# Kernel optimization log

Measured on AMD Instinct MI355X. Metric: run time of the kernel, lower is better.

The kernel has to match this reference:

```python
import jax, jax.numpy as jnp
import numpy as np

D_MODEL = 1024
SEQ_LEN = 32768


def setup_inputs() -> dict:
    key = jax.random.key(0)
    k1, k2, k3 = jax.random.split(key, 3)
    inputs = jax.random.normal(k1, (SEQ_LEN,), dtype=jnp.float32)
    W = jax.random.normal(k2, (D_MODEL, D_MODEL), dtype=jnp.float32) * (1.0 / np.sqrt(D_MODEL))
    b = jax.random.normal(k3, (D_MODEL,), dtype=jnp.float32) * 0.01
    return {"inputs": inputs, "W": W, "b": b}


def reference(inputs, W, b):
    d_model = W.shape[0]
    # t: [D], p: [L] -- log(1 + position)
    t = jnp.linspace(0.0, 1.0, d_model, dtype=inputs.dtype)
    p = jnp.log1p(jnp.arange(inputs.shape[0], dtype=inputs.dtype))
    # phase[l, d] = 2*pi * inputs[l] * (t[d] + p[l]); sum sin over positions
    phase = 2.0 * jnp.pi * inputs[:, None] * (t[None, :] + p[:, None])  # [L, D]
    signal = jnp.sum(jnp.sin(phase), axis=0)  # [D]
    # nn.Linear: x @ W.T + b
    return signal @ W.T + b
```

## Files before the change

### kernel.cpp

```cpp
#include <hip/hip_runtime.h>

#define L_TOTAL 32768
#define D_MODEL 1024
#define CHUNK   128
#define BLOCKS_A (L_TOTAL / CHUNK)

__global__ __launch_bounds__(1024) void signal_kernel(const float* __restrict__ x,
                                                      float* __restrict__ signal) {
    __shared__ float2 sxp[CHUNK];
    const int tid  = threadIdx.x;
    const int base = blockIdx.x * CHUNK;
    if (tid < CHUNK) {
        const float xv = x[base + tid];
        const float pv = __logf(1.0f + (float)(base + tid));
        sxp[tid] = make_float2(xv, xv * pv);
    }
    __syncthreads();

    const float t = (float)tid * (1.0f / 1023.0f);
    float a = 0.f;
    #pragma unroll 8
    for (int il = 0; il < CHUNK; ++il) {
        const float2 v = sxp[il];
        const float g = __builtin_amdgcn_fractf(fmaf(v.x, t, v.y));
        a += __builtin_amdgcn_sinf(g);
    }
    atomicAdd(&signal[tid], a);
}

__global__ __launch_bounds__(256) void matvec_kernel(const float* __restrict__ W,
                                                     const float* __restrict__ b,
                                                     const float* __restrict__ signal,
                                                     float* __restrict__ out) {
    const int wave = threadIdx.x >> 6;
    const int lane = threadIdx.x & 63;
    const int row  = blockIdx.x * 4 + wave;

    const float4* Wr = (const float4*)(W + (size_t)row * D_MODEL);
    const float4* S  = (const float4*)signal;

    float sum = 0.f;
    #pragma unroll
    for (int k = 0; k < 4; ++k) {
        const float4 w4 = Wr[lane + 64 * k];
        const float4 s4 = S[lane + 64 * k];
        sum += w4.x * s4.x + w4.y * s4.y + w4.z * s4.z + w4.w * s4.w;
    }
    #pragma unroll
    for (int off = 32; off > 0; off >>= 1)
        sum += __shfl_down(sum, off, 64);
    if (lane == 0) out[row] = sum + b[row];
}

extern "C" void kernel_launch(void* const* d_in, const int* in_sizes, int n_in,
                              void* d_out, int out_size, void* d_ws, size_t ws_size,
                              hipStream_t stream) {
    const float* x = (const float*)d_in[0];
    const float* W = (const float*)d_in[1];
    const float* b = (const float*)d_in[2];
    float* out    = (float*)d_out;
    float* signal = (float*)d_ws;

    hipMemsetAsync(signal, 0, D_MODEL * sizeof(float), stream);
    signal_kernel<<<BLOCKS_A, 1024, 0, stream>>>(x, signal);
    matvec_kernel<<<D_MODEL / 4, 256, 0, stream>>>(W, b, signal, out);
}
```

Measured before the change: 73.48 us.

## Fuse signal and matvec into one cooperative kernel partitioned by output column

Replaces the memset, the atomic-accumulating signal kernel and the separate matvec kernel with a single cooperative kernel. Each block owns 4 output dimensions and loops over the whole sequence, so the sum needs no atomics, and grid syncs hand the signal vector to the matvec phase through the output buffer. The goal is to remove launch overhead and atomic contention. In exchange, every block recomputes log1p for all positions, two grid-wide barriers are added, and only 4 dims per block limits the parallel work.

```diff
diff --git a/kernel.cpp b/kernel.cpp
--- a/kernel.cpp
+++ b/kernel.cpp
@@ -1,55 +1,89 @@
 #include <hip/hip_runtime.h>
+#include <hip/hip_cooperative_groups.h>
+
+namespace cg = cooperative_groups;
 
 #define L_TOTAL 32768
 #define D_MODEL 1024
-#define CHUNK   128
-#define BLOCKS_A (L_TOTAL / CHUNK)
+#define NBLK    256
+#define NTHR    1024
+#define CL      4096
+#define NCHUNK  (L_TOTAL / CL)
+#define JITER   (CL / 256)
 
-__global__ __launch_bounds__(1024) void signal_kernel(const float* __restrict__ x,
-                                                      float* __restrict__ signal) {
-    __shared__ float2 sxp[CHUNK];
+__global__ __launch_bounds__(NTHR, 4) void fused_kernel(const float* __restrict__ x,
+                                                        const float* __restrict__ W,
+                                                        const float* __restrict__ b,
+                                                        float* __restrict__ out) {
+    __shared__ float2 sxp[CL];
+    __shared__ float  ssig[D_MODEL];
+    __shared__ float  wsum[64];
+    __shared__ float  rsum[16];
+
     const int tid  = threadIdx.x;
-    const int base = blockIdx.x * CHUNK;
-    if (tid < CHUNK) {
-        const float xv = x[base + tid];
-        const float pv = __logf(1.0f + (float)(base + tid));
-        sxp[tid] = make_float2(xv, xv * pv);
+    const int blk  = blockIdx.x;
+    const int lane = tid & 63;
+    const int wv   = tid >> 6;
+    const int di   = tid & 3;
+    const int li   = tid >> 2;
+    const float t  = (float)(blk * 4 + di) * (1.0f / 1023.0f);
+
+    float a = 0.f;
+    for (int c = 0; c < NCHUNK; ++c) {
+        const int cbase = c * CL;
+        __syncthreads();
+        #pragma unroll
+        for (int s = 0; s < CL / NTHR; ++s) {
+            const int idx = tid + s * NTHR;
+            const int l   = cbase + idx;
+            const float xv = x[l];
+            sxp[idx] = make_float2(xv, xv * __logf(1.0f + (float)l));
+        }
+        __syncthreads();
+        #pragma unroll
+        for (int j = 0; j < JITER; ++j) {
+            const float2 v = sxp[li + 256 * j];
+            const float g = __builtin_amdgcn_fractf(fmaf(v.x, t, v.y));
+            a += __builtin_amdgcn_sinf(g);
+        }
     }
+    a += __shfl_xor(a, 4, 64);
+    a += __shfl_xor(a, 8, 64);
+    a += __shfl_xor(a, 16, 64);
+    a += __shfl_xor(a, 32, 64);
+    if (lane < 4) wsum[wv * 4 + lane] = a;
     __syncthreads();
+    if (tid < 64) {
+        float v = wsum[tid];
+        v += __shfl_xor(v, 4, 64);
+        v += __shfl_xor(v, 8, 64);
+        v += __shfl_xor(v, 16, 64);
+        v += __shfl_xor(v, 32, 64);
+        if (tid < 4) out[blk * 4 + tid] = v;
+    }
 
-    const float t = (float)tid * (1.0f / 1023.0f);
-    float a = 0.f;
-    #pragma unroll 8
-    for (int il = 0; il < CHUNK; ++il) {
-        const float2 v = sxp[il];
-        const float g = __builtin_amdgcn_fractf(fmaf(v.x, t, v.y));
-        a += __builtin_amdgcn_sinf(g);
-    }
-    atomicAdd(&signal[tid], a);
-}
+    cg::this_grid().sync();
 
-__global__ __launch_bounds__(256) void matvec_kernel(const float* __restrict__ W,
-                                                     const float* __restrict__ b,
-                                                     const float* __restrict__ signal,
-                                                     float* __restrict__ out) {
-    const int wave = threadIdx.x >> 6;
-    const int lane = threadIdx.x & 63;
-    const int row  = blockIdx.x * 4 + wave;
+    ssig[tid] = out[tid];
 
-    const float4* Wr = (const float4*)(W + (size_t)row * D_MODEL);
-    const float4* S  = (const float4*)signal;
+    cg::this_grid().sync();
 
-    float sum = 0.f;
-    #pragma unroll
-    for (int k = 0; k < 4; ++k) {
-        const float4 w4 = Wr[lane + 64 * k];
-        const float4 s4 = S[lane + 64 * k];
-        sum += w4.x * s4.x + w4.y * s4.y + w4.z * s4.z + w4.w * s4.w;
-    }
+    const int r4  = tid >> 8;
+    const int cc  = tid & 255;
+    const int row = blk * 4 + r4;
+    const float4 w4 = ((const float4*)(W + (size_t)row * D_MODEL))[cc];
+    const float4 s4 = ((const float4*)ssig)[cc];
+    float sum = w4.x * s4.x + w4.y * s4.y + w4.z * s4.z + w4.w * s4.w;
     #pragma unroll
     for (int off = 32; off > 0; off >>= 1)
         sum += __shfl_down(sum, off, 64);
-    if (lane == 0) out[row] = sum + b[row];
+    if (lane == 0) rsum[wv] = sum;
+    __syncthreads();
+    if (tid < 4) {
+        const int r = blk * 4 + tid;
+        out[r] = rsum[tid * 4] + rsum[tid * 4 + 1] + rsum[tid * 4 + 2]
+               + rsum[tid * 4 + 3] + b[r];
+    }
 }
 
 extern "C" void kernel_launch(void* const* d_in, const int* in_sizes, int n_in,
@@ -58,10 +92,8 @@
     const float* x = (const float*)d_in[0];
     const float* W = (const float*)d_in[1];
     const float* b = (const float*)d_in[2];
-    float* out    = (float*)d_out;
-    float* signal = (float*)d_ws;
-
-    hipMemsetAsync(signal, 0, D_MODEL * sizeof(float), stream);
-    signal_kernel<<<BLOCKS_A, 1024, 0, stream>>>(x, signal);
-    matvec_kernel<<<D_MODEL / 4, 256, 0, stream>>>(W, b, signal, out);
+    float* out     = (float*)d_out;
+    void* args[] = { (void*)&x, (void*)&W, (void*)&b, (void*)&out };
+    hipLaunchCooperativeKernel((const void*)fused_kernel, dim3(NBLK), dim3(NTHR),
+                               args, 0, stream);
 }
```

Result: slower. 113.3 us (+54.2%).

## Split signal kernel into smaller blocks over d-quarters with multiple accumulators

Applied to the files above, without the earlier changes.

Reorganizes the signal kernel grid from 1024-thread blocks covering all d over 128 positions to 256-thread blocks covering a quarter of d over 64 positions, giving many more blocks to fill the GPU. The inner loop uses four independent accumulators to break the serial add chain. This doubles the number of global atomic adds into the signal buffer.

```diff
diff --git a/kernel.cpp b/kernel.cpp
--- a/kernel.cpp
+++ b/kernel.cpp
@@ -2,30 +2,41 @@
 
 #define L_TOTAL 32768
 #define D_MODEL 1024
-#define CHUNK   128
-#define BLOCKS_A (L_TOTAL / CHUNK)
+#define LCHUNK  64
+#define NQ      (D_MODEL / 256)
+#define NBLK_S  ((L_TOTAL / LCHUNK) * NQ)
 
-__global__ __launch_bounds__(1024) void signal_kernel(const float* __restrict__ x,
-                                                      float* __restrict__ signal) {
-    __shared__ float2 sxp[CHUNK];
-    const int tid  = threadIdx.x;
-    const int base = blockIdx.x * CHUNK;
-    if (tid < CHUNK) {
-        const float xv = x[base + tid];
-        const float pv = __logf(1.0f + (float)(base + tid));
-        sxp[tid] = make_float2(xv, xv * pv);
+__global__ __launch_bounds__(256) void signal_kernel(const float* __restrict__ x,
+                                                     float* __restrict__ signal) {
+    __shared__ float2 sxp[LCHUNK];
+    const int tid   = threadIdx.x;
+    const int q     = blockIdx.x & (NQ - 1);
+    const int c     = blockIdx.x >> 2;
+    const int lbase = c * LCHUNK;
+
+    if (tid < LCHUNK) {
+        const int l   = lbase + tid;
+        const float xv = x[l];
+        sxp[tid] = make_float2(xv, xv * __logf(1.0f + (float)l));
     }
     __syncthreads();
 
-    const float t = (float)tid * (1.0f / 1023.0f);
-    float a = 0.f;
-    #pragma unroll 8
-    for (int il = 0; il < CHUNK; ++il) {
-        const float2 v = sxp[il];
-        const float g = __builtin_amdgcn_fractf(fmaf(v.x, t, v.y));
-        a += __builtin_amdgcn_sinf(g);
+    const int   d = q * 256 + tid;
+    const float t = (float)d * (1.0f / 1023.0f);
+
+    float a0 = 0.f, a1 = 0.f, a2 = 0.f, a3 = 0.f;
+    #pragma unroll
+    for (int j = 0; j < LCHUNK; j += 4) {
+        const float2 v0 = sxp[j + 0];
+        const float2 v1 = sxp[j + 1];
+        const float2 v2 = sxp[j + 2];
+        const float2 v3 = sxp[j + 3];
+        a0 += __builtin_amdgcn_sinf(__builtin_amdgcn_fractf(fmaf(v0.x, t, v0.y)));
+        a1 += __builtin_amdgcn_sinf(__builtin_amdgcn_fractf(fmaf(v1.x, t, v1.y)));
+        a2 += __builtin_amdgcn_sinf(__builtin_amdgcn_fractf(fmaf(v2.x, t, v2.y)));
+        a3 += __builtin_amdgcn_sinf(__builtin_amdgcn_fractf(fmaf(v3.x, t, v3.y)));
     }
-    atomicAdd(&signal[tid], a);
+    atomicAdd(&signal[d], (a0 + a1) + (a2 + a3));
 }
 
 __global__ __launch_bounds__(256) void matvec_kernel(const float* __restrict__ W,
@@ -62,6 +73,6 @@
     float* signal = (float*)d_ws;
 
     hipMemsetAsync(signal, 0, D_MODEL * sizeof(float), stream);
-    signal_kernel<<<BLOCKS_A, 1024, 0, stream>>>(x, signal);
+    signal_kernel<<<NBLK_S, 256, 0, stream>>>(x, signal);
     matvec_kernel<<<D_MODEL / 4, 256, 0, stream>>>(W, b, signal, out);
 }
```

Measured after the change: 76.57 us. 4.2% more time.
